# Kernel optimization log

Measured on AMD Instinct MI355X. Metric: run time of the kernel, lower is better.

## Reference

```python
import jax, jax.numpy as jnp
import numpy as np

# Fixed Gauss-Legendre quadrature on [-A, A] replacing scipy.integrate.quadrature
A = 5.0
NQ = 64
_x, _w = np.polynomial.legendre.leggauss(NQ)
GL_X = jnp.asarray(_x * A, dtype=jnp.float32)  # nodes scaled to [-5, 5]
# Fold exp(-z^2/2)/sqrt(2*pi) and interval scaling into the weights
GL_W_EFF = jnp.asarray(_w * A * np.exp(-(_x * A) ** 2 / 2.0) / np.sqrt(2.0 * np.pi), dtype=jnp.float32)

# given_params=True constants
SIG_M1, SIG_M2, SIG_I = 1.0, 1.0, 1.0
SIG_M1N1, SIG_M2N2 = 1.0, 0.5
SIG_N1I, SIG_N2I = 0.5, 1.9
SIG_M1W, SIG_M2W = 2.8, -2.2
TAU, DT = 100.0, 20.0


def setup_inputs() -> dict:
    key = jax.random.key(0)
    B, T = 8192, 2048
    u = jax.random.normal(key, (B, T), dtype=jnp.float32)
    return {"u": u}


def reference(u):
    B, T = u.shape
    alpha = jnp.float32(DT / TAU)

    def step(carry, u_t):
        k1, k2, v = carry  # each [B]
        delta = jnp.sqrt(SIG_M1**2 * k1**2 + SIG_M2**2 * k2**2 + SIG_I**2 * u_t**2)  # [B]
        # gauss_int[b] = int_{-A}^{A} (1 - tanh(delta_b z)^2) exp(-z^2/2) dz / sqrt(2pi)
        dphi = 1.0 - jnp.tanh(delta[:, None] * GL_X[None, :]) ** 2  # [B, NQ]
        gauss_int = dphi @ GL_W_EFF  # [B]
        k1_new = k1 + (-k1 + SIG_M1N1 * gauss_int * k1 + SIG_N1I * gauss_int * v) * alpha
        k2_new = k2 + (-k2 + SIG_M2N2 * gauss_int * k2 + SIG_N2I * gauss_int * v) * alpha
        v_new = v + (-v + u_t) * alpha
        z = SIG_M1W * k1_new + SIG_M2W * k2_new
        return (k1_new, k2_new, v_new), z

    zeros = jnp.zeros((B,), dtype=u.dtype)
    _, z_seq = jax.lax.scan(step, (zeros, zeros, zeros), u.T)  # z_seq: [T, B]
    # z_hist: [B, T+1], column 0 is the zero initial state
    z_hist = jnp.concatenate([zeros[:, None], z_seq.T], axis=1)
    return z_hist
```

## Files before the change

### kernel.cpp

```cpp
#include <hip/hip_runtime.h>
#include <math.h>


#define Bsz   8192
#define Tlen  2048
#define TP1   2049
#define NQ    64
#define NG    2049
#define NTAB2 2048
#define INV_H 32.0f
#define CHUNKS 16
#define CLEN  128
#define WARM  128
#define BLOCK 256
#define SIM_GRID 512

#define WS_TAB 128

__global__ __launch_bounds__(256) void setup_kernel(float* __restrict__ ws,
                                                    float* __restrict__ out) {
    __shared__ float  fx[NQ], fw[NQ];
    __shared__ double inv[NQ + 1];
    const int tid = threadIdx.x;
    if (tid <= NQ) inv[tid] = (tid == 0) ? 0.0 : 1.0 / (double)tid;
    __syncthreads();
    if (tid < NQ) {
        double z = cos(3.14159265358979323846 * (tid + 0.75) / (NQ + 0.5));
        double p1 = 1.0, p2 = 0.0, pp = 1.0;
        for (int it = 0; it < 4; ++it) {
            p1 = 1.0; p2 = 0.0;
            for (int j = 1; j <= NQ; ++j) {
                double p3 = p2; p2 = p1;
                p1 = ((2.0 * j - 1.0) * z * p2 - (j - 1.0) * p3) * inv[j];
            }
            pp = NQ * (z * p1 - p2) / (z * z - 1.0);
            if (it < 3) z -= p1 / pp;
        }
        double w  = 2.0 / ((1.0 - z * z) * pp * pp);
        double xs = z * 5.0;
        fx[tid] = (float)xs;
        fw[tid] = (float)(w * 5.0 * exp(-0.5 * xs * xs) * 0.3989422804014327);
    }
    __syncthreads();
    const int j = blockIdx.x * BLOCK + tid;
    if (j < NG) {
        const float d = sqrtf((float)j * (1.0f / INV_H));
        float acc = 0.0f;
        #pragma unroll 8
        for (int q = 0; q < NQ; ++q) {
            float t = tanhf(d * fx[q]);
            acc = fmaf(fw[q], 1.0f - t * t, acc);
        }
        ws[WS_TAB + j] = acc;
    }
    out[(size_t)j * TP1] = 0.0f;
}

__device__ __forceinline__ float step_one(float uu, float& k1, float& k2,
                                          float& v, const float2* s_tab) {
    float s   = fmaf(k1, k1, fmaf(k2, k2, uu * uu));
    float idx = fminf(s * INV_H, 2046.999f);
    int   i0  = (int)idx;
    float f   = idx - (float)i0;
    float2 g2 = s_tab[i0];
    float g   = fmaf(f, g2.y - g2.x, g2.x);
    float gv  = g * v;
    float nk1 = fmaf(k1, fmaf(0.2f, g, 0.8f), 0.10f * gv);
    float nk2 = fmaf(k2, fmaf(0.1f, g, 0.8f), 0.38f * gv);
    v  = fmaf(0.2f, uu - v, v);
    k1 = nk1; k2 = nk2;
    return fmaf(2.8f, nk1, -2.2f * nk2);
}

__global__ __launch_bounds__(BLOCK, 3) void sim_kernel(const float* __restrict__ u,
                                                       const float* __restrict__ ws,
                                                       float* __restrict__ out) {
    __shared__ float2 s_tab[NTAB2];
    __shared__ float2 s_u2[4][BLOCK];
    __shared__ float  s_zt[64 * 65];
    const int tid = threadIdx.x;

    {
        const float* g = ws + WS_TAB;
        #pragma unroll
        for (int i = 0; i < NTAB2 / (BLOCK * 4); ++i) {
            int k = (i * BLOCK + tid) * 4;
            float4 a = *(const float4*)(g + k);
            float  b = g[k + 4];
            s_tab[k + 0] = make_float2(a.x, a.y);
            s_tab[k + 1] = make_float2(a.y, a.z);
            s_tab[k + 2] = make_float2(a.z, a.w);
            s_tab[k + 3] = make_float2(a.w, b);
        }
    }

    const int c    = blockIdx.x >> 5;
    const int bb   = blockIdx.x & 31;
    const int rowb = bb * BLOCK;
    const int t_out   = c * CLEN;
    const int t_begin = (c == 0) ? 0 : (t_out - WARM);

    float k1 = 0.f, k2 = 0.f, v = 0.f;
    const int r1 = tid >> 1;
    const int h4 = (tid & 1) * 4;
    const int ph = (tid & 1) * 2;
    const float* __restrict__ upb = u + (size_t)(rowb + r1) * Tlen + h4;

    float4 Ua = *(const float4*)(upb + t_begin);
    float4 Ub = *(const float4*)(upb + t_begin + 128 * Tlen);

    for (int tb = t_begin; tb < t_out; tb += 8) {
        __syncthreads();
        s_u2[ph    ][r1      ] = make_float2(Ua.x, Ua.y);
        s_u2[ph + 1][r1      ] = make_float2(Ua.z, Ua.w);
        s_u2[ph    ][r1 + 128] = make_float2(Ub.x, Ub.y);
        s_u2[ph + 1][r1 + 128] = make_float2(Ub.z, Ub.w);
        const int tn = tb + 8;
        Ua = *(const float4*)(upb + tn);
        Ub = *(const float4*)(upb + tn + 128 * Tlen);
        __syncthreads();
        #pragma unroll
        for (int p = 0; p < 4; ++p) {
            float2 uu = s_u2[p][tid];
            step_one(uu.x, k1, k2, v, s_tab);
            step_one(uu.y, k1, k2, v, s_tab);
        }
    }

    const int myw = tid >> 6;
    const int lr  = tid & 63;
    for (int h = 0; h < 2; ++h) {
        float zz[64];
        #pragma unroll
        for (int gq = 0; gq < 8; ++gq) {
            const int tb = t_out + h * 64 + gq * 8;
            __syncthreads();
            s_u2[ph    ][r1      ] = make_float2(Ua.x, Ua.y);
            s_u2[ph + 1][r1      ] = make_float2(Ua.z, Ua.w);
            s_u2[ph    ][r1 + 128] = make_float2(Ub.x, Ub.y);
            s_u2[ph + 1][r1 + 128] = make_float2(Ub.z, Ub.w);
            int tn = tb + 8;
            if (tn > Tlen - 8) tn = Tlen - 8;
            Ua = *(const float4*)(upb + tn);
            Ub = *(const float4*)(upb + tn + 128 * Tlen);
            __syncthreads();
            #pragma unroll
            for (int p = 0; p < 4; ++p) {
                float2 uu = s_u2[p][tid];
                zz[gq * 8 + 2 * p    ] = step_one(uu.x, k1, k2, v, s_tab);
                zz[gq * 8 + 2 * p + 1] = step_one(uu.y, k1, k2, v, s_tab);
            }
        }
        const int cb = t_out + 1 + h * 64;
        for (int p4 = 0; p4 < 4; ++p4) {
            __syncthreads();
            if (myw == p4) {
                #pragma unroll
                for (int j = 0; j < 64; ++j)
                    s_zt[lr * 65 + j] = zz[j];
            }
            __syncthreads();
            #pragma unroll
            for (int k = 0; k < 16; ++k) {
                int d   = tid + 256 * k;
                int row = d >> 6;
                int col = d & 63;
                out[(size_t)(rowb + p4 * 64 + row) * TP1 + cb + col] =
                    s_zt[row * 65 + col];
            }
        }
    }
}

extern "C" void kernel_launch(void* const* d_in, const int* in_sizes, int n_in,
                              void* d_out, int out_size, void* d_ws, size_t ws_size,
                              hipStream_t stream) {
    const float* u = (const float*)d_in[0];
    float* out = (float*)d_out;
    float* ws  = (float*)d_ws;
    setup_kernel<<<32, BLOCK, 0, stream>>>(ws, out);
    sim_kernel<<<SIM_GRID, BLOCK, 0, stream>>>(u, ws, out);
}
```

Baseline: 152.5 us.

## Halve time-chunk length, double grid, and double-buffer the input staging

The time axis is split into 32 chunks of 64 steps instead of 16 chunks of 128. The grid doubles to 1024 blocks, and launch bounds now allow 4 blocks per CU. The aim is to shorten each block's serial recurrence and raise occupancy to hide latency in the latency-bound scan. The input staging buffer becomes double-buffered, which drops one barrier per 8-step group, and the transpose scratch reuses that buffer to cut LDS use. The cost is more redundant warm-up work, since every chunk still recomputes up to 128 warm-up steps, and chunk 1 now warms up over only 64 steps, which could affect accuracy.

```diff
diff --git a/kernel.cpp b/kernel.cpp
--- a/kernel.cpp
+++ b/kernel.cpp
@@ -9,11 +9,11 @@
 #define NG    2049
 #define NTAB2 2048
 #define INV_H 32.0f
-#define CHUNKS 16
-#define CLEN  128
+#define CHUNKS 32
+#define CLEN  64
 #define WARM  128
 #define BLOCK 256
-#define SIM_GRID 512
+#define SIM_GRID 1024
 
 #define WS_TAB 128
 
@@ -72,12 +72,11 @@
     return fmaf(2.8f, nk1, -2.2f * nk2);
 }
 
-__global__ __launch_bounds__(BLOCK, 3) void sim_kernel(const float* __restrict__ u,
+__global__ __launch_bounds__(BLOCK, 4) void sim_kernel(const float* __restrict__ u,
                                                        const float* __restrict__ ws,
                                                        float* __restrict__ out) {
     __shared__ float2 s_tab[NTAB2];
-    __shared__ float2 s_u2[4][BLOCK];
-    __shared__ float  s_zt[64 * 65];
+    __shared__ float2 s_ub[2048];
     const int tid = threadIdx.x;
 
     {
@@ -98,7 +97,7 @@
     const int bb   = blockIdx.x & 31;
     const int rowb = bb * BLOCK;
     const int t_out   = c * CLEN;
-    const int t_begin = (c == 0) ? 0 : (t_out - WARM);
+    const int t_begin = (t_out >= WARM) ? (t_out - WARM) : 0;
 
     float k1 = 0.f, k2 = 0.f, v = 0.f;
     const int r1 = tid >> 1;
@@ -108,66 +107,66 @@
 
     float4 Ua = *(const float4*)(upb + t_begin);
     float4 Ub = *(const float4*)(upb + t_begin + 128 * Tlen);
+    int gi = 0;
 
-    for (int tb = t_begin; tb < t_out; tb += 8) {
-        __syncthreads();
-        s_u2[ph    ][r1      ] = make_float2(Ua.x, Ua.y);
-        s_u2[ph + 1][r1      ] = make_float2(Ua.z, Ua.w);
-        s_u2[ph    ][r1 + 128] = make_float2(Ub.x, Ub.y);
-        s_u2[ph + 1][r1 + 128] = make_float2(Ub.z, Ub.w);
+    for (int tb = t_begin; tb < t_out; tb += 8, ++gi) {
+        float2* ut = s_ub + (gi & 1) * 1024;
+        ut[ ph      * BLOCK + r1      ] = make_float2(Ua.x, Ua.y);
+        ut[(ph + 1) * BLOCK + r1      ] = make_float2(Ua.z, Ua.w);
+        ut[ ph      * BLOCK + r1 + 128] = make_float2(Ub.x, Ub.y);
+        ut[(ph + 1) * BLOCK + r1 + 128] = make_float2(Ub.z, Ub.w);
         const int tn = tb + 8;
         Ua = *(const float4*)(upb + tn);
         Ub = *(const float4*)(upb + tn + 128 * Tlen);
         __syncthreads();
         #pragma unroll
         for (int p = 0; p < 4; ++p) {
-            float2 uu = s_u2[p][tid];
+            float2 uu = ut[p * BLOCK + tid];
             step_one(uu.x, k1, k2, v, s_tab);
             step_one(uu.y, k1, k2, v, s_tab);
         }
     }
 
-    const int myw = tid >> 6;
-    const int lr  = tid & 63;
-    for (int h = 0; h < 2; ++h) {
-        float zz[64];
+    float zz[CLEN];
+    #pragma unroll
+    for (int gq = 0; gq < 8; ++gq, ++gi) {
+        const int tb = t_out + gq * 8;
+        float2* ut = s_ub + (gi & 1) * 1024;
+        ut[ ph      * BLOCK + r1      ] = make_float2(Ua.x, Ua.y);
+        ut[(ph + 1) * BLOCK + r1      ] = make_float2(Ua.z, Ua.w);
+        ut[ ph      * BLOCK + r1 + 128] = make_float2(Ub.x, Ub.y);
+        ut[(ph + 1) * BLOCK + r1 + 128] = make_float2(Ub.z, Ub.w);
+        int tn = tb + 8;
+        if (tn > Tlen - 8) tn = Tlen - 8;
+        Ua = *(const float4*)(upb + tn);
+        Ub = *(const float4*)(upb + tn + 128 * Tlen);
+        __syncthreads();
         #pragma unroll
-        for (int gq = 0; gq < 8; ++gq) {
-            const int tb = t_out + h * 64 + gq * 8;
-            __syncthreads();
-            s_u2[ph    ][r1      ] = make_float2(Ua.x, Ua.y);
-            s_u2[ph + 1][r1      ] = make_float2(Ua.z, Ua.w);
-            s_u2[ph    ][r1 + 128] = make_float2(Ub.x, Ub.y);
-            s_u2[ph + 1][r1 + 128] = make_float2(Ub.z, Ub.w);
-            int tn = tb + 8;
-            if (tn > Tlen - 8) tn = Tlen - 8;
-            Ua = *(const float4*)(upb + tn);
-            Ub = *(const float4*)(upb + tn + 128 * Tlen);
-            __syncthreads();
+        for (int p = 0; p < 4; ++p) {
+            float2 uu = ut[p * BLOCK + tid];
+            zz[gq * 8 + 2 * p    ] = step_one(uu.x, k1, k2, v, s_tab);
+            zz[gq * 8 + 2 * p + 1] = step_one(uu.y, k1, k2, v, s_tab);
+        }
+    }
+
+    float* s_zt = (float*)s_ub;
+    const int cb = t_out + 1;
+    const int lr = tid & 31;
+    for (int p4 = 0; p4 < 8; ++p4) {
+        __syncthreads();
+        if ((tid >> 5) == p4) {
             #pragma unroll
-            for (int p = 0; p < 4; ++p) {
-                float2 uu = s_u2[p][tid];
-                zz[gq * 8 + 2 * p    ] = step_one(uu.x, k1, k2, v, s_tab);
-                zz[gq * 8 + 2 * p + 1] = step_one(uu.y, k1, k2, v, s_tab);
-            }
+            for (int j = 0; j < 64; ++j)
+                s_zt[lr * 65 + j] = zz[j];
         }
-        const int cb = t_out + 1 + h * 64;
-        for (int p4 = 0; p4 < 4; ++p4) {
-            __syncthreads();
-            if (myw == p4) {
-                #pragma unroll
-                for (int j = 0; j < 64; ++j)
-                    s_zt[lr * 65 + j] = zz[j];
-            }
-            __syncthreads();
-            #pragma unroll
-            for (int k = 0; k < 16; ++k) {
-                int d   = tid + 256 * k;
-                int row = d >> 6;
-                int col = d & 63;
-                out[(size_t)(rowb + p4 * 64 + row) * TP1 + cb + col] =
-                    s_zt[row * 65 + col];
-            }
+        __syncthreads();
+        #pragma unroll
+        for (int k = 0; k < 8; ++k) {
+            int d   = tid + 256 * k;
+            int row = d >> 6;
+            int col = d & 63;
+            out[(size_t)(rowb + p4 * 32 + row) * TP1 + cb + col] =
+                s_zt[row * 65 + col];
         }
     }
 }
```

Result: slower. 166.1 us (+8.9%).
